# Performance work log

Measured on AMD Instinct MI355X. Metric: run time of the kernel, lower is better.

Reference implementation:

```python
import jax, jax.numpy as jnp
import numpy as np

B, T, F = 32, 2048, 1
U = 256          # enc_units
L = 3            # layer_depth
H4 = 4 * U       # gates i,f,g,o (keras LSTMCell order)


def setup_inputs() -> dict:
    key = jax.random.key(0)
    ks = jax.random.split(key, 14)
    g = lambda k, s, sc=0.05: (jax.random.normal(k, s, dtype=jnp.float32) * sc)
    inp = {
        "inputs": jax.random.normal(ks[0], (B, T, F), dtype=jnp.float32),
        # layer 0 (input dim F), forward + backward directions
        "W0f": g(ks[1], (F, H4)), "U0f": g(ks[2], (U, H4)), "b0f": g(ks[3], (H4,)),
        "W0b": g(ks[4], (F, H4)), "U0b": g(ks[5], (U, H4)), "b0b": g(ks[6], (H4,)),
        # layers 1..L-1 (input dim 2U), stacked on leading axis
        "Wf": g(ks[7], (L - 1, 2 * U, H4)), "Uf": g(ks[8], (L - 1, U, H4)), "bf": g(ks[9], (L - 1, H4)),
        "Wb": g(ks[10], (L - 1, 2 * U, H4)), "Ub": g(ks[11], (L - 1, U, H4)), "bb": g(ks[12], (L - 1, H4)),
    }
    return inp


def _lstm(x_btf, W, Uw, b, h0, c0):
    """Single-direction LSTM over time. x_btf: [B,T,Fin]. Returns seq [B,T,U], hT, cT."""
    # precompute input projection for all steps: [T,B,4U]
    xz = jnp.einsum('btf,fh->tbh', x_btf, W) + b

    def step(carry, z_in):
        h, c = carry
        z = z_in + h @ Uw                      # [B,4U]
        i, f, g_, o = jnp.split(z, 4, axis=-1)  # keras gate order i,f,c,o
        c = jax.nn.sigmoid(f) * c + jax.nn.sigmoid(i) * jnp.tanh(g_)
        h = jax.nn.sigmoid(o) * jnp.tanh(c)
        return (h, c), h

    (hT, cT), hs = jax.lax.scan(step, (h0, c0), xz)
    return jnp.swapaxes(hs, 0, 1), hT, cT       # [B,T,U]


def _bidir(x, Wf_, Uf_, bf_, Wb_, Ub_, bb_, states):
    bsz = x.shape[0]
    if states is None:
        z = jnp.zeros((bsz, U), dtype=x.dtype)
        h0f = c0f = h0b = c0b = z
    else:
        h0f, c0f, h0b, c0b = states  # keras Bidirectional state order
    out_f, hf, cf = _lstm(x, Wf_, Uf_, bf_, h0f, c0f)
    out_b, hb, cb = _lstm(x[:, ::-1], Wb_, Ub_, bb_, h0b, c0b)
    out_b = out_b[:, ::-1]  # re-align backward outputs with time axis
    return jnp.concatenate([out_f, out_b], axis=-1), (hf, cf, hb, cb)


def reference(inputs, W0f, U0f, b0f, W0b, U0b, b0b, Wf, Uf, bf, Wb, Ub, bb):
    out, states = _bidir(inputs, W0f, U0f, b0f, W0b, U0b, b0b, None)
    for l in range(L - 1):
        out, states = _bidir(out, Wf[l], Uf[l], bf[l], Wb[l], Ub[l], bb[l], states)
    return out, states
```

## Files before the change

kernel.cpp:

```cpp
#include <hip/hip_runtime.h>
#include <stdint.h>


typedef unsigned short u16;
typedef unsigned int   u32;
typedef unsigned long long u64;
typedef __attribute__((ext_vector_type(8)))  short short8;
typedef __attribute__((ext_vector_type(16))) float f32x16;

#define B_   32
#define T_   2048
#define U_   256
#define H4_  1024
#define CHUNK 256
#define FLAG_STRIDE 16

__device__ __forceinline__ float bf2f(u16 v){ u32 u = ((u32)v) << 16; return __builtin_bit_cast(float, u); }
__device__ __forceinline__ u16 f2bf(float f){
  u32 u = __builtin_bit_cast(u32, f);
  u32 r = (u + 0x7FFFu + ((u >> 16) & 1u)) >> 16;
  return (u16)r;
}
__device__ __forceinline__ float sigm(float x){
  return __builtin_amdgcn_rcpf(1.f + __builtin_amdgcn_exp2f(-1.4426950408889634f * x));
}
__device__ __forceinline__ float tanh_(float x){
  x = fminf(fmaxf(x, -30.f), 30.f);
  float t = __builtin_amdgcn_exp2f(2.8853900817779268f * x);
  return (t - 1.f) * __builtin_amdgcn_rcpf(t + 1.f);
}

__device__ __forceinline__ void gl2lds16(const void* g, void* s){
  __builtin_amdgcn_global_load_lds(
      (const __attribute__((address_space(1))) u32*)(uintptr_t)g,
      (__attribute__((address_space(3))) u32*)(u32)(uintptr_t)s, 16, 0, 0);
}

__global__ void prep_upack(const float* __restrict__ U0f, const float* __restrict__ U0b,
                           const float* __restrict__ Uf,  const float* __restrict__ Ub,
                           u16* __restrict__ upack)
{
  int e = blockIdx.x * 256 + threadIdx.x;
  int j     = e & 7;
  int l     = (e >> 3) & 63;
  int kt    = (e >> 9) & 15;
  int w     = (e >> 13) & 3;
  int g     = (e >> 15) & 7;
  int dir   = (e >> 18) & 1;
  int layer = e >> 19;
  int colg = w * 256 + g * 32 + (l & 31);
  int k    = kt * 16 + ((l >> 5) & 1) * 8 + j;
  const float* src;
  if (layer == 0) src = dir ? U0b : U0f;
  else            src = (dir ? Ub : Uf) + (size_t)(layer - 1) * (U_ * H4_);
  upack[e] = f2bf(src[(size_t)k * H4_ + colg]);
}

__global__ void prep_wt(const float* __restrict__ Wf, const float* __restrict__ Wb,
                        u16* __restrict__ wt)
{
  int e = blockIdx.x * 256 + threadIdx.x;
  int k    = e & 511;
  int colg = (e >> 9) & 1023;
  int ld   = e >> 19;
  int layer = ld >> 1, dir = ld & 1;
  const float* src = (dir ? Wb : Wf) + (size_t)layer * (512 * H4_);
  wt[e] = f2bf(src[(size_t)k * H4_ + colg]);
}

__global__ void ws_fail(float* o){ o[0] = -1.0e6f; }

__global__ __launch_bounds__(256) void xz_gemm(
    const u16* __restrict__ xs,
    const u16* __restrict__ wt,
    const float* __restrict__ bf_,
    const float* __restrict__ bb_,
    u16* __restrict__ xz,
    int layer, int s0)
{
  const int bm = blockIdx.x;
  const int bn = blockIdx.y;
  const int dir = blockIdx.z;
  const int tid = threadIdx.x, w = tid >> 6, l = tid & 63;
  const int wm = w >> 1, wn = w & 1;
  __shared__ u16 As[128 * 64];
  __shared__ u16 Bs[128 * 64];
  const u16* wpanel = wt + (size_t)((layer - 1) * 2 + dir) * (H4_ * 512);
  const float* bias = (dir ? bb_ : bf_) + (size_t)(layer - 1) * H4_;
  f32x16 acc00{}, acc01{}, acc10{}, acc11{};

  for (int k0 = 0; k0 < 8; k0++){
    #pragma unroll
    for (int i = 0; i < 4; i++){
      int inst = i * 4 + w;
      int R = bm * 128 + inst * 8 + (l >> 3);
      int sl = R >> 5, b = R & 31;
      int t = dir ? (T_ - 1 - (s0 + sl)) : (s0 + sl);
      const u16* g = xs + ((size_t)(t * 32 + b) * 512 + k0 * 64 + (l & 7) * 8);
      gl2lds16(g, (void*)(As + inst * 512));
    }
    #pragma unroll
    for (int i = 0; i < 4; i++){
      int inst = i * 4 + w;
      int colg = bn * 128 + inst * 8 + (l >> 3);
      const u16* g = wpanel + ((size_t)colg * 512 + k0 * 64 + (l & 7) * 8);
      gl2lds16(g, (void*)(Bs + inst * 512));
    }
    asm volatile("s_waitcnt vmcnt(0)" ::: "memory");
    __syncthreads();
    #pragma unroll
    for (int kt = 0; kt < 4; kt++){
      int ko = kt * 16 + (l >> 5) * 8;
      short8 a0 = *(const short8*)(As + (wm * 64 +      (l & 31)) * 64 + ko);
      short8 a1 = *(const short8*)(As + (wm * 64 + 32 + (l & 31)) * 64 + ko);
      short8 b0 = *(const short8*)(Bs + (wn * 64 +      (l & 31)) * 64 + ko);
      short8 b1 = *(const short8*)(Bs + (wn * 64 + 32 + (l & 31)) * 64 + ko);
      acc00 = __builtin_amdgcn_mfma_f32_32x32x16_bf16(a0, b0, acc00, 0, 0, 0);
      acc01 = __builtin_amdgcn_mfma_f32_32x32x16_bf16(a0, b1, acc01, 0, 0, 0);
      acc10 = __builtin_amdgcn_mfma_f32_32x32x16_bf16(a1, b0, acc10, 0, 0, 0);
      acc11 = __builtin_amdgcn_mfma_f32_32x32x16_bf16(a1, b1, acc11, 0, 0, 0);
    }
    __syncthreads();
  }
  const int lrow = 4 * (l >> 5);
  auto epi = [&](const f32x16& A, int mi, int ni){
    int colg = bn * 128 + wn * 64 + ni * 32 + (l & 31);
    float bv = bias[colg];
    #pragma unroll
    for (int r = 0; r < 16; r++){
      int row = wm * 64 + mi * 32 + (r & 3) + 8 * (r >> 2) + lrow;
      int R = bm * 128 + row;
      int sl = R >> 5, b = R & 31;
      xz[((size_t)(dir * CHUNK + sl) * 32 + b) * 1024 + colg] = f2bf(A[r] + bv);
    }
  };
  epi(acc00, 0, 0); epi(acc01, 0, 1); epi(acc10, 1, 0); epi(acc11, 1, 1);
}

__global__ __launch_bounds__(256) void rec_step(
    int layer, int s0, int nsteps,
    const float* __restrict__ x_in,
    const float* __restrict__ w0f, const float* __restrict__ w0b,
    const float* __restrict__ b0f, const float* __restrict__ b0b,
    const u16* __restrict__ upack,
    const u16* __restrict__ xz,
    u16*  __restrict__ xseq_out,
    float* __restrict__ dout,
    u16*  __restrict__ h_buf,
    float* __restrict__ state_c,
    u32*  __restrict__ flags)
{
  const int bid = blockIdx.x;
  const int dir = bid >> 3, g = bid & 7;
  const int tid = threadIdx.x, w = tid >> 6, l = tid & 63;
  __shared__ u16 h_st[8192];
  __shared__ float z_lds[32 * 132];

  short8 Bf[16];
  {
    const u16* up = upack + (size_t)((((layer * 2 + dir) * 8 + g) * 4 + w) * 16) * 512 + l * 8;
    #pragma unroll
    for (int kt = 0; kt < 16; kt++) Bf[kt] = *(const short8*)(up + kt * 512);
  }
  const int b = tid & 31, ug = tid >> 5;
  const int u0 = g * 32 + ug * 4;
  float c[4];
  #pragma unroll
  for (int i = 0; i < 4; i++) c[i] = state_c[dir * 8192 + b * 256 + u0 + i];
  float w0v[4][4], bia[4][4];
  if (layer == 0){
    const float* W0 = dir ? w0b : w0f;
    const float* B0 = dir ? b0b : b0f;
    #pragma unroll
    for (int gt = 0; gt < 4; gt++)
      #pragma unroll
      for (int i = 0; i < 4; i++){
        w0v[gt][i] = W0[gt * 256 + u0 + i];
        bia[gt][i] = B0[gt * 256 + u0 + i];
      }
  }
  u16* hb  = h_buf + dir * 2 * 8192;
  u32* flg = flags + (layer * 2 + dir) * (8 * FLAG_STRIDE);

  for (int ss = 0; ss < nsteps; ss++){
    const int s = s0 + ss;
    const int t = dir ? (T_ - 1 - s) : s;

    float xv = 0.f; uint2 xq0, xq1, xq2, xq3;
    if (layer == 0){
      xv = x_in[b * T_ + t];
    } else {
      const u16* xp = xz + ((size_t)(dir * CHUNK + ss) * 32 + b) * 1024 + u0;
      xq0 = *(const uint2*)(xp);
      xq1 = *(const uint2*)(xp + 256);
      xq2 = *(const uint2*)(xp + 512);
      xq3 = *(const uint2*)(xp + 768);
    }

    if (w == 0 && l < 8){
      while (__hip_atomic_load(&flg[l * FLAG_STRIDE], __ATOMIC_ACQUIRE,
                               __HIP_MEMORY_SCOPE_AGENT) < (u32)s) {}
    }
    __syncthreads();

    {
      const u16* hsrc = hb + (s & 1) * 8192;
      #pragma unroll
      for (int i = 0; i < 4; i++){
        int inst = i * 4 + w;
        gl2lds16(hsrc + inst * 512 + l * 8, (void*)(h_st + inst * 512));
      }
    }
    asm volatile("s_waitcnt vmcnt(0)" ::: "memory");
    __syncthreads();

    f32x16 acc{};
    #pragma unroll
    for (int kt = 0; kt < 16; kt++){
      short8 a = *(const short8*)(h_st + kt * 512 + l * 8);
      acc = __builtin_amdgcn_mfma_f32_32x32x16_bf16(a, Bf[kt], acc, 0, 0, 0);
    }
    {
      int cb = w * 32 + (l & 31);
      #pragma unroll
      for (int r = 0; r < 16; r++){
        int row = (r & 3) + 8 * (r >> 2) + 4 * (l >> 5);
        z_lds[row * 132 + cb] = acc[r];
      }
    }
    __syncthreads();

    float hv[4];
    #pragma unroll
    for (int i = 0; i < 4; i++){
      float zi = z_lds[b * 132 +       ug * 4 + i];
      float zf = z_lds[b * 132 + 32  + ug * 4 + i];
      float zg = z_lds[b * 132 + 64  + ug * 4 + i];
      float zo = z_lds[b * 132 + 96  + ug * 4 + i];
      if (layer == 0){
        zi += xv * w0v[0][i] + bia[0][i];
        zf += xv * w0v[1][i] + bia[1][i];
        zg += xv * w0v[2][i] + bia[2][i];
        zo += xv * w0v[3][i] + bia[3][i];
      } else {
        zi += bf2f(((const u16*)&xq0)[i]);
        zf += bf2f(((const u16*)&xq1)[i]);
        zg += bf2f(((const u16*)&xq2)[i]);
        zo += bf2f(((const u16*)&xq3)[i]);
      }
      float si = sigm(zi), sf = sigm(zf), so = sigm(zo);
      c[i] = sf * c[i] + si * tanh_(zg);
      hv[i] = so * tanh_(c[i]);
    }

    u32 plo = (u32)f2bf(hv[0]) | ((u32)f2bf(hv[1]) << 16);
    u32 phi = (u32)f2bf(hv[2]) | ((u32)f2bf(hv[3]) << 16);
    {
      u64 hp = (u64)plo | ((u64)phi << 32);
      int F = (u0 >> 4) * 512 + ((u0 >> 3) & 1) * 256 + b * 8 + (u0 & 7);
      __hip_atomic_store((u64*)(hb + ((s + 1) & 1) * 8192 + F), hp,
                         __ATOMIC_RELAXED, __HIP_MEMORY_SCOPE_AGENT);
    }
    if (layer < 2){
      *(uint2*)(xseq_out + (size_t)(t * 32 + b) * 512 + dir * 256 + u0) = make_uint2(plo, phi);
    } else {
      *(float4*)(dout + ((size_t)(b * T_ + t) * 512 + dir * 256 + u0)) =
          make_float4(hv[0], hv[1], hv[2], hv[3]);
    }
    if (ss == nsteps - 1){
      #pragma unroll
      for (int i = 0; i < 4; i++) state_c[dir * 8192 + b * 256 + u0 + i] = c[i];
      if (layer == 2 && s == T_ - 1){
        size_t sb = (size_t)B_ * T_ * 512;
        #pragma unroll
        for (int i = 0; i < 4; i++){
          dout[sb + (size_t)(dir * 2 + 0) * 8192 + b * 256 + u0 + i] = hv[i];
          dout[sb + (size_t)(dir * 2 + 1) * 8192 + b * 256 + u0 + i] = c[i];
        }
      }
    }
    asm volatile("s_waitcnt vmcnt(0)" ::: "memory");
    __syncthreads();
    if (tid == 0)
      __hip_atomic_store(&flg[g * FLAG_STRIDE], (u32)(s + 1),
                         __ATOMIC_RELAXED, __HIP_MEMORY_SCOPE_AGENT);
  }
}

extern "C" void kernel_launch(void* const* d_in, const int* in_sizes, int n_in,
                              void* d_out, int out_size, void* d_ws, size_t ws_size,
                              hipStream_t stream)
{
  const float* x   = (const float*)d_in[0];
  const float* W0f = (const float*)d_in[1];
  const float* U0f = (const float*)d_in[2];
  const float* b0f = (const float*)d_in[3];
  const float* W0b = (const float*)d_in[4];
  const float* U0b = (const float*)d_in[5];
  const float* b0b = (const float*)d_in[6];
  const float* Wf  = (const float*)d_in[7];
  const float* Uf  = (const float*)d_in[8];
  const float* bf_ = (const float*)d_in[9];
  const float* Wb  = (const float*)d_in[10];
  const float* Ub  = (const float*)d_in[11];
  const float* bb_ = (const float*)d_in[12];
  float* out = (float*)d_out;

  char* base = (char*)d_ws;
  size_t off = 0;
  auto carve = [&](size_t bytes) -> char* {
    char* r = base + off;
    off += (bytes + 255) & ~(size_t)255;
    return r;
  };
  u16* xs0   = (u16*)carve((size_t)T_ * 32 * 512 * 2);
  u16* xs1   = (u16*)carve((size_t)T_ * 32 * 512 * 2);
  u16* xzbuf = (u16*)carve((size_t)2 * CHUNK * 32 * 1024 * 2);
  u16* upack = (u16*)carve((size_t)1572864 * 2);
  u16* wt    = (u16*)carve((size_t)2097152 * 2);
  u16* hbuf  = (u16*)carve((size_t)2 * 2 * 8192 * 2);
  float* stc = (float*)carve((size_t)2 * 8192 * 4);
  u32* flags = (u32*)carve((size_t)3 * 2 * 8 * FLAG_STRIDE * 4);
  if (off > ws_size){
    ws_fail<<<1, 1, 0, stream>>>(out);
    return;
  }
  size_t zbytes = (size_t)((char*)(flags + 3 * 2 * 8 * FLAG_STRIDE) - (char*)hbuf);
  hipMemsetAsync(hbuf, 0, zbytes, stream);

  prep_upack<<<6144, 256, 0, stream>>>(U0f, U0b, Uf, Ub, upack);
  prep_wt<<<8192, 256, 0, stream>>>(Wf, Wb, wt);

  rec_step<<<16, 256, 0, stream>>>(0, 0, T_, x, W0f, W0b, b0f, b0b,
                                   upack, nullptr, xs0, nullptr, hbuf, stc, flags);
  for (int layer = 1; layer <= 2; layer++){
    const u16* xsrc = (layer == 1) ? xs0 : xs1;
    u16* xdst = (layer == 1) ? xs1 : nullptr;
    for (int pch = 0; pch < T_ / CHUNK; pch++){
      xz_gemm<<<dim3(CHUNK * 32 / 128, H4_ / 128, 2), 256, 0, stream>>>(
          xsrc, wt, bf_, bb_, xzbuf, layer, pch * CHUNK);
      rec_step<<<16, 256, 0, stream>>>(layer, pch * CHUNK, CHUNK,
                                       nullptr, nullptr, nullptr, nullptr, nullptr,
                                       upack, xzbuf, xdst,
                                       (layer == 2) ? out : nullptr,
                                       hbuf, stc, flags);
    }
  }
}
```

Baseline: 19.11 ms.

## Replace block-level flag sync with per-wave tagged ring buffer for LSTM recurrence

Restructures the recurrent kernel so that each wave owns 8 hidden units across all four gates and exchanges h through a tagged 8-slot ring in global memory. Each 64-bit entry carries the step number, so consumers poll the data itself and no longer need per-block flags or block-wide barriers. Gate-interleaved column packing for U and for the xz GEMM output lets each wave compute all of its gates locally, and the input projection is seeded straight into the MFMA accumulator. Producers are throttled with a read-progress counter checked every four steps, which adds polling traffic and relies on relaxed atomics being ordered correctly.

Result: slower. 32.91 ms (+72.2%).

```diff
diff --git a/kernel.cpp b/kernel.cpp
--- a/kernel.cpp
+++ b/kernel.cpp
@@ -6,20 +6,18 @@
 typedef unsigned int   u32;
 typedef unsigned long long u64;
 typedef __attribute__((ext_vector_type(8)))  short short8;
+typedef __attribute__((ext_vector_type(4)))  u32  u32x4;
 typedef __attribute__((ext_vector_type(16))) float f32x16;
 
-#define B_   32
-#define T_   2048
-#define U_   256
-#define H4_  1024
+#define B_    32
+#define T_    2048
 #define CHUNK 256
-#define FLAG_STRIDE 16
+#define RING  8
 
 __device__ __forceinline__ float bf2f(u16 v){ u32 u = ((u32)v) << 16; return __builtin_bit_cast(float, u); }
 __device__ __forceinline__ u16 f2bf(float f){
   u32 u = __builtin_bit_cast(u32, f);
-  u32 r = (u + 0x7FFFu + ((u >> 16) & 1u)) >> 16;
-  return (u16)r;
+  return (u16)((u + 0x7FFFu + ((u >> 16) & 1u)) >> 16);
 }
 __device__ __forceinline__ float sigm(float x){
   return __builtin_amdgcn_rcpf(1.f + __builtin_amdgcn_exp2f(-1.4426950408889634f * x));
@@ -41,19 +39,18 @@
                            u16* __restrict__ upack)
 {
   int e = blockIdx.x * 256 + threadIdx.x;
-  int j     = e & 7;
-  int l     = (e >> 3) & 63;
-  int kt    = (e >> 9) & 15;
-  int w     = (e >> 13) & 3;
-  int g     = (e >> 15) & 7;
+  int j  = e & 7;
+  int l  = (e >> 3) & 63;
+  int kt = (e >> 9) & 15;
+  int w  = (e >> 13) & 31;
   int dir   = (e >> 18) & 1;
   int layer = e >> 19;
-  int colg = w * 256 + g * 32 + (l & 31);
+  int cc   = l & 31;
+  int colg = (cc >> 3) * 256 + w * 8 + (cc & 7);
   int k    = kt * 16 + ((l >> 5) & 1) * 8 + j;
-  const float* src;
-  if (layer == 0) src = dir ? U0b : U0f;
-  else            src = (dir ? Ub : Uf) + (size_t)(layer - 1) * (U_ * H4_);
-  upack[e] = f2bf(src[(size_t)k * H4_ + colg]);
+  const float* src = (layer == 0) ? (dir ? U0b : U0f)
+                                  : ((dir ? Ub : Uf) + (size_t)(layer - 1) * (256 * 1024));
+  upack[e] = f2bf(src[(size_t)k * 1024 + colg]);
 }
 
 __global__ void prep_wt(const float* __restrict__ Wf, const float* __restrict__ Wb,
@@ -64,8 +61,16 @@
   int colg = (e >> 9) & 1023;
   int ld   = e >> 19;
   int layer = ld >> 1, dir = ld & 1;
-  const float* src = (dir ? Wb : Wf) + (size_t)layer * (512 * H4_);
-  wt[e] = f2bf(src[(size_t)k * H4_ + colg]);
+  const float* src = (dir ? Wb : Wf) + (size_t)layer * (512 * 1024);
+  wt[e] = f2bf(src[(size_t)k * 1024 + colg]);
+}
+
+__global__ void prep_xT(const float* __restrict__ x, float* __restrict__ xT)
+{
+  int e = blockIdx.x * 256 + threadIdx.x;
+  int t = e >> 5, pos = e & 31;
+  int b = (pos & 3) + 8 * ((pos >> 2) & 3) + 4 * (pos >> 4);
+  xT[t * 32 + pos] = x[(size_t)b * T_ + t];
 }
 
 __global__ void ws_fail(float* o){ o[0] = -1.0e6f; }
@@ -85,8 +90,8 @@
   const int wm = w >> 1, wn = w & 1;
   __shared__ u16 As[128 * 64];
   __shared__ u16 Bs[128 * 64];
-  const u16* wpanel = wt + (size_t)((layer - 1) * 2 + dir) * (H4_ * 512);
-  const float* bias = (dir ? bb_ : bf_) + (size_t)(layer - 1) * H4_;
+  const u16* wpanel = wt + (size_t)((layer - 1) * 2 + dir) * (1024 * 512);
+  const float* bias = (dir ? bb_ : bf_) + (size_t)(layer - 1) * 1024;
   f32x16 acc00{}, acc01{}, acc10{}, acc11{};
 
   for (int k0 = 0; k0 < 8; k0++){
@@ -126,165 +131,207 @@
   auto epi = [&](const f32x16& A, int mi, int ni){
     int colg = bn * 128 + wn * 64 + ni * 32 + (l & 31);
     float bv = bias[colg];
+    int unit = colg & 255, gate = colg >> 8;
+    int vcol = (unit >> 3) * 32 + gate * 8 + (unit & 7);
     #pragma unroll
     for (int r = 0; r < 16; r++){
       int row = wm * 64 + mi * 32 + (r & 3) + 8 * (r >> 2) + lrow;
       int R = bm * 128 + row;
       int sl = R >> 5, b = R & 31;
-      xz[((size_t)(dir * CHUNK + sl) * 32 + b) * 1024 + colg] = f2bf(A[r] + bv);
+      int pos = (b & 3) + ((b >> 3) & 3) * 4 + ((b >> 2) & 1) * 16;
+      xz[((size_t)(dir * CHUNK + sl) * 1024 + vcol) * 32 + pos] = f2bf(A[r] + bv);
     }
   };
   epi(acc00, 0, 0); epi(acc01, 0, 1); epi(acc10, 1, 0); epi(acc11, 1, 1);
 }
 
-__global__ __launch_bounds__(256) void rec_step(
+__global__ __launch_bounds__(256, 1) void rec_wave(
     int layer, int s0, int nsteps,
-    const float* __restrict__ x_in,
+    const float* __restrict__ xT,
     const float* __restrict__ w0f, const float* __restrict__ w0b,
     const float* __restrict__ b0f, const float* __restrict__ b0b,
     const u16* __restrict__ upack,
     const u16* __restrict__ xz,
     u16*  __restrict__ xseq_out,
     float* __restrict__ dout,
-    u16*  __restrict__ h_buf,
+    u64*  __restrict__ ring,
     float* __restrict__ state_c,
-    u32*  __restrict__ flags)
-{
-  const int bid = blockIdx.x;
-  const int dir = bid >> 3, g = bid & 7;
-  const int tid = threadIdx.x, w = tid >> 6, l = tid & 63;
-  __shared__ u16 h_st[8192];
-  __shared__ float z_lds[32 * 132];
+    int*  __restrict__ rawp)
+{
+  const int tid = threadIdx.x;
+  const int wid = tid >> 6, l = tid & 63;
+  const int dir = blockIdx.x >> 3;
+  const int w   = (blockIdx.x & 7) * 4 + wid;
+  const int role = dir * 32 + w;
+  const int c = l & 31, half = l >> 5;
+  const int g = c >> 3, uu = c & 7;
+  const int unit = w * 8 + uu;
+  const int b0 = g * 8 + half * 4;
+
+  __shared__ float zt[4][32 * 33];
+  float* myz = zt[wid];
 
   short8 Bf[16];
-  {
-    const u16* up = upack + (size_t)((((layer * 2 + dir) * 8 + g) * 4 + w) * 16) * 512 + l * 8;
-    #pragma unroll
-    for (int kt = 0; kt < 16; kt++) Bf[kt] = *(const short8*)(up + kt * 512);
-  }
-  const int b = tid & 31, ug = tid >> 5;
-  const int u0 = g * 32 + ug * 4;
-  float c[4];
   #pragma unroll
-  for (int i = 0; i < 4; i++) c[i] = state_c[dir * 8192 + b * 256 + u0 + i];
-  float w0v[4][4], bia[4][4];
+  for (int kt = 0; kt < 16; kt++)
+    Bf[kt] = *(const short8*)(upack +
+        ((size_t)((((layer * 2 + dir) * 32 + w) * 16 + kt) * 64 + l)) * 8);
+
+  float cst[4];
+  #pragma unroll
+  for (int i = 0; i < 4; i++)
+    cst[i] = state_c[(dir * 256 + unit) * 32 + b0 + i];
+
+  float w0v = 0.f, b0v = 0.f;
   if (layer == 0){
     const float* W0 = dir ? w0b : w0f;
-    const float* B0 = dir ? b0b : b0f;
-    #pragma unroll
-    for (int gt = 0; gt < 4; gt++)
-      #pragma unroll
-      for (int i = 0; i < 4; i++){
-        w0v[gt][i] = W0[gt * 256 + u0 + i];
-        bia[gt][i] = B0[gt * 256 + u0 + i];
-      }
-  }
-  u16* hb  = h_buf + dir * 2 * 8192;
-  u32* flg = flags + (layer * 2 + dir) * (8 * FLAG_STRIDE);
+    const float* Bb = dir ? b0b : b0f;
+    int colg = g * 256 + unit;
+    w0v = W0[colg]; b0v = Bb[colg];
+  }
+
+  u64* myring = ring + (size_t)dir * RING * 4096;
 
   for (int ss = 0; ss < nsteps; ss++){
     const int s = s0 + ss;
+    const int G = layer * T_ + s;
     const int t = dir ? (T_ - 1 - s) : s;
 
-    float xv = 0.f; uint2 xq0, xq1, xq2, xq3;
+    f32x16 acce{}, acco{};
     if (layer == 0){
-      xv = x_in[b * T_ + t];
+      const float4* xp = (const float4*)(xT + t * 32 + half * 16);
+      float4 x0 = xp[0], x1 = xp[1], x2 = xp[2], x3 = xp[3];
+      float xv[16] = {x0.x,x0.y,x0.z,x0.w, x1.x,x1.y,x1.z,x1.w,
+                      x2.x,x2.y,x2.z,x2.w, x3.x,x3.y,x3.z,x3.w};
+      #pragma unroll
+      for (int r = 0; r < 16; r++) acce[r] = xv[r] * w0v + b0v;
     } else {
-      const u16* xp = xz + ((size_t)(dir * CHUNK + ss) * 32 + b) * 1024 + u0;
-      xq0 = *(const uint2*)(xp);
-      xq1 = *(const uint2*)(xp + 256);
-      xq2 = *(const uint2*)(xp + 512);
-      xq3 = *(const uint2*)(xp + 768);
-    }
-
-    if (w == 0 && l < 8){
-      while (__hip_atomic_load(&flg[l * FLAG_STRIDE], __ATOMIC_ACQUIRE,
-                               __HIP_MEMORY_SCOPE_AGENT) < (u32)s) {}
-    }
-    __syncthreads();
-
-    {
-      const u16* hsrc = hb + (s & 1) * 8192;
+      const u16* xp = xz + ((size_t)((dir * CHUNK + ss) * 1024 + w * 32 + c)) * 32 + half * 16;
+      short8 xa = *(const short8*)xp;
+      short8 xb = *(const short8*)(xp + 8);
+      #pragma unroll
+      for (int r = 0; r < 8; r++){ acce[r] = bf2f((u16)xa[r]); acce[r + 8] = bf2f((u16)xb[r]); }
+    }
+
+    u64* slotr = myring + (size_t)(G & 7) * 4096;
+
+    if (l < 32){
+      const u64* cw = slotr + l * 129;
+      while ((u32)(__hip_atomic_load(cw, __ATOMIC_RELAXED, __HIP_MEMORY_SCOPE_AGENT) >> 32)
+             != (u32)G) {}
+    }
+
+    u32x4 alo[16];
+    bool ok;
+    do {
+      u32 bad = 0;
+      #pragma unroll
+      for (int kt = 0; kt < 16; kt++){
+        u64 v0 = __hip_atomic_load(slotr + (kt * 8 + half * 4 + 0) * 32 + c,
+                                   __ATOMIC_RELAXED, __HIP_MEMORY_SCOPE_AGENT);
+        u64 v1 = __hip_atomic_load(slotr + (kt * 8 + half * 4 + 1) * 32 + c,
+                                   __ATOMIC_RELAXED, __HIP_MEMORY_SCOPE_AGENT);
+        u64 v2 = __hip_atomic_load(slotr + (kt * 8 + half * 4 + 2) * 32 + c,
+                                   __ATOMIC_RELAXED, __HIP_MEMORY_SCOPE_AGENT);
+        u64 v3 = __hip_atomic_load(slotr + (kt * 8 + half * 4 + 3) * 32 + c,
+                                   __ATOMIC_RELAXED, __HIP_MEMORY_SCOPE_AGENT);
+        alo[kt] = (u32x4){ (u32)v0, (u32)v1, (u32)v2, (u32)v3 };
+        bad |= ((u32)(v0 >> 32) ^ (u32)G) | ((u32)(v1 >> 32) ^ (u32)G)
+             | ((u32)(v2 >> 32) ^ (u32)G) | ((u32)(v3 >> 32) ^ (u32)G);
+      }
+      ok = (__ballot(bad != 0) == 0);
+    } while (!ok);
+
+    if (l == 0)
+      __hip_atomic_store(&rawp[role], G + 1, __ATOMIC_RELAXED, __HIP_MEMORY_SCOPE_AGENT);
+
+    #pragma unroll
+    for (int kt = 0; kt < 16; kt++){
+      short8 A = __builtin_bit_cast(short8, alo[kt]);
+      if (kt & 1) acco = __builtin_amdgcn_mfma_f32_32x32x16_bf16(A, Bf[kt], acco, 0, 0, 0);
+      else        acce = __builtin_amdgcn_mfma_f32_32x32x16_bf16(A, Bf[kt], acce, 0, 0, 0);
+    }
+
+    #pragma unroll
+    for (int r = 0; r < 16; r++){
+      int row = (r & 3) + 8 * (r >> 2) + 4 * half;
+      myz[row * 33 + c] = acce[r] + acco[r];
+    }
+    float zq[4][4];
+    #pragma unroll
+    for (int gg = 0; gg < 4; gg++)
+      #pragma unroll
+      for (int i = 0; i < 4; i++)
+        zq[gg][i] = myz[(b0 + i) * 33 + gg * 8 + uu];
+
+    float hv[4];
+    #pragma unroll
+    for (int i = 0; i < 4; i++){
+      float si = sigm(zq[0][i]);
+      float sf = sigm(zq[1][i]);
+      float tg = tanh_(zq[2][i]);
+      float so = sigm(zq[3][i]);
+      cst[i] = sf * cst[i] + si * tg;
+      hv[i]  = so * tanh_(cst[i]);
+    }
+
+    if ((G & 3) == 0){
+      int need = G - 3;
+      bool bok;
+      do {
+        int v = 0x7fffffff;
+        if (l < 32)
+          v = __hip_atomic_load(&rawp[dir * 32 + l], __ATOMIC_RELAXED, __HIP_MEMORY_SCOPE_AGENT);
+        bok = (__ballot(v < need) == 0);
+      } while (!bok);
+    }
+
+    float hpv[4];
+    #pragma unroll
+    for (int i = 0; i < 4; i++) hpv[i] = __shfl_xor(hv[i], 1);
+    const int odd = uu & 1;
+    const int p = w * 4 + (uu >> 1);
+    u64* slotw = myring + (size_t)((G + 1) & 7) * 4096;
+    float lo_f[2], hi_f[2];
+    u32 hpk[2];
+    #pragma unroll
+    for (int k2 = 0; k2 < 2; k2++){
+      int i = odd * 2 + k2;
+      lo_f[k2] = odd ? hpv[i] : hv[i];
+      hi_f[k2] = odd ? hv[i] : hpv[i];
+      hpk[k2]  = (u32)f2bf(lo_f[k2]) | ((u32)f2bf(hi_f[k2]) << 16);
+    }
+    #pragma unroll
+    for (int k2 = 0; k2 < 2; k2++){
+      int i = odd * 2 + k2;
+      __hip_atomic_store(slotw + p * 32 + (b0 + i),
+                         (u64)hpk[k2] | ((u64)(u32)(G + 1) << 32),
+                         __ATOMIC_RELAXED, __HIP_MEMORY_SCOPE_AGENT);
+    }
+    #pragma unroll
+    for (int k2 = 0; k2 < 2; k2++){
+      int i = odd * 2 + k2;
+      if (layer < 2){
+        *(u32*)(xseq_out + (size_t)(t * 32 + b0 + i) * 512 + dir * 256 + w * 8 + (uu & ~1)) = hpk[k2];
+      } else {
+        *(float2*)(dout + ((size_t)(b0 + i) * T_ + t) * 512 + dir * 256 + w * 8 + (uu & ~1)) =
+            make_float2(lo_f[k2], hi_f[k2]);
+      }
+    }
+
+    if (layer == 2 && s == T_ - 1){
+      size_t sb = (size_t)B_ * T_ * 512;
       #pragma unroll
       for (int i = 0; i < 4; i++){
-        int inst = i * 4 + w;
-        gl2lds16(hsrc + inst * 512 + l * 8, (void*)(h_st + inst * 512));
+        dout[sb + (size_t)dir * 16384 +        (b0 + i) * 256 + unit] = hv[i];
+        dout[sb + (size_t)dir * 16384 + 8192 + (b0 + i) * 256 + unit] = cst[i];
       }
     }
-    asm volatile("s_waitcnt vmcnt(0)" ::: "memory");
-    __syncthreads();
-
-    f32x16 acc{};
-    #pragma unroll
-    for (int kt = 0; kt < 16; kt++){
-      short8 a = *(const short8*)(h_st + kt * 512 + l * 8);
-      acc = __builtin_amdgcn_mfma_f32_32x32x16_bf16(a, Bf[kt], acc, 0, 0, 0);
-    }
-    {
-      int cb = w * 32 + (l & 31);
-      #pragma unroll
-      for (int r = 0; r < 16; r++){
-        int row = (r & 3) + 8 * (r >> 2) + 4 * (l >> 5);
-        z_lds[row * 132 + cb] = acc[r];
-      }
-    }
-    __syncthreads();
-
-    float hv[4];
-    #pragma unroll
-    for (int i = 0; i < 4; i++){
-      float zi = z_lds[b * 132 +       ug * 4 + i];
-      float zf = z_lds[b * 132 + 32  + ug * 4 + i];
-      float zg = z_lds[b * 132 + 64  + ug * 4 + i];
-      float zo = z_lds[b * 132 + 96  + ug * 4 + i];
-      if (layer == 0){
-        zi += xv * w0v[0][i] + bia[0][i];
-        zf += xv * w0v[1][i] + bia[1][i];
-        zg += xv * w0v[2][i] + bia[2][i];
-        zo += xv * w0v[3][i] + bia[3][i];
-      } else {
-        zi += bf2f(((const u16*)&xq0)[i]);
-        zf += bf2f(((const u16*)&xq1)[i]);
-        zg += bf2f(((const u16*)&xq2)[i]);
-        zo += bf2f(((const u16*)&xq3)[i]);
-      }
-      float si = sigm(zi), sf = sigm(zf), so = sigm(zo);
-      c[i] = sf * c[i] + si * tanh_(zg);
-      hv[i] = so * tanh_(c[i]);
-    }
-
-    u32 plo = (u32)f2bf(hv[0]) | ((u32)f2bf(hv[1]) << 16);
-    u32 phi = (u32)f2bf(hv[2]) | ((u32)f2bf(hv[3]) << 16);
-    {
-      u64 hp = (u64)plo | ((u64)phi << 32);
-      int F = (u0 >> 4) * 512 + ((u0 >> 3) & 1) * 256 + b * 8 + (u0 & 7);
-      __hip_atomic_store((u64*)(hb + ((s + 1) & 1) * 8192 + F), hp,
-                         __ATOMIC_RELAXED, __HIP_MEMORY_SCOPE_AGENT);
-    }
-    if (layer < 2){
-      *(uint2*)(xseq_out + (size_t)(t * 32 + b) * 512 + dir * 256 + u0) = make_uint2(plo, phi);
-    } else {
-      *(float4*)(dout + ((size_t)(b * T_ + t) * 512 + dir * 256 + u0)) =
-          make_float4(hv[0], hv[1], hv[2], hv[3]);
-    }
-    if (ss == nsteps - 1){
-      #pragma unroll
-      for (int i = 0; i < 4; i++) state_c[dir * 8192 + b * 256 + u0 + i] = c[i];
-      if (layer == 2 && s == T_ - 1){
-        size_t sb = (size_t)B_ * T_ * 512;
-        #pragma unroll
-        for (int i = 0; i < 4; i++){
-          dout[sb + (size_t)(dir * 2 + 0) * 8192 + b * 256 + u0 + i] = hv[i];
-          dout[sb + (size_t)(dir * 2 + 1) * 8192 + b * 256 + u0 + i] = c[i];
-        }
-      }
-    }
-    asm volatile("s_waitcnt vmcnt(0)" ::: "memory");
-    __syncthreads();
-    if (tid == 0)
-      __hip_atomic_store(&flg[g * FLAG_STRIDE], (u32)(s + 1),
-                         __ATOMIC_RELAXED, __HIP_MEMORY_SCOPE_AGENT);
-  }
+  }
+
+  #pragma unroll
+  for (int i = 0; i < 4; i++)
+    state_c[(dir * 256 + unit) * 32 + b0 + i] = cst[i];
 }
 
 extern "C" void kernel_launch(void* const* d_in, const int* in_sizes, int n_in,
@@ -315,35 +362,37 @@
   };
   u16* xs0   = (u16*)carve((size_t)T_ * 32 * 512 * 2);
   u16* xs1   = (u16*)carve((size_t)T_ * 32 * 512 * 2);
-  u16* xzbuf = (u16*)carve((size_t)2 * CHUNK * 32 * 1024 * 2);
+  u16* xzbuf = (u16*)carve((size_t)2 * CHUNK * 1024 * 32 * 2);
   u16* upack = (u16*)carve((size_t)1572864 * 2);
   u16* wt    = (u16*)carve((size_t)2097152 * 2);
-  u16* hbuf  = (u16*)carve((size_t)2 * 2 * 8192 * 2);
-  float* stc = (float*)carve((size_t)2 * 8192 * 4);
-  u32* flags = (u32*)carve((size_t)3 * 2 * 8 * FLAG_STRIDE * 4);
+  float* xT  = (float*)carve((size_t)T_ * 32 * 4);
+  u64* ring  = (u64*)carve((size_t)2 * RING * 4096 * 8);
+  float* stc = (float*)carve((size_t)2 * 256 * 32 * 4);
+  int* rawp  = (int*)carve((size_t)64 * 4);
+  char* zend = base + off;
   if (off > ws_size){
     ws_fail<<<1, 1, 0, stream>>>(out);
     return;
   }
-  size_t zbytes = (size_t)((char*)(flags + 3 * 2 * 8 * FLAG_STRIDE) - (char*)hbuf);
-  hipMemsetAsync(hbuf, 0, zbytes, stream);
+  hipMemsetAsync(ring, 0, (size_t)(zend - (char*)ring), stream);
 
   prep_upack<<<6144, 256, 0, stream>>>(U0f, U0b, Uf, Ub, upack);
   prep_wt<<<8192, 256, 0, stream>>>(Wf, Wb, wt);
-
-  rec_step<<<16, 256, 0, stream>>>(0, 0, T_, x, W0f, W0b, b0f, b0b,
-                                   upack, nullptr, xs0, nullptr, hbuf, stc, flags);
+  prep_xT<<<256, 256, 0, stream>>>(x, xT);
+
+  rec_wave<<<16, 256, 0, stream>>>(0, 0, T_, xT, W0f, W0b, b0f, b0b,
+                                   upack, nullptr, xs0, nullptr, ring, stc, rawp);
   for (int layer = 1; layer <= 2; layer++){
     const u16* xsrc = (layer == 1) ? xs0 : xs1;
     u16* xdst = (layer == 1) ? xs1 : nullptr;
     for (int pch = 0; pch < T_ / CHUNK; pch++){
-      xz_gemm<<<dim3(CHUNK * 32 / 128, H4_ / 128, 2), 256, 0, stream>>>(
+      xz_gemm<<<dim3(CHUNK * 32 / 128, 8, 2), 256, 0, stream>>>(
           xsrc, wt, bf_, bb_, xzbuf, layer, pch * CHUNK);
-      rec_step<<<16, 256, 0, stream>>>(layer, pch * CHUNK, CHUNK,
+      rec_wave<<<16, 256, 0, stream>>>(layer, pch * CHUNK, CHUNK,
                                        nullptr, nullptr, nullptr, nullptr, nullptr,
                                        upack, xzbuf, xdst,
                                        (layer == 2) ? out : nullptr,
-                                       hbuf, stc, flags);
-    }
-  }
-}
+                                       ring, stc, rawp);
+    }
+  }
+}
```
